# Kernel tuning notes

Hardware: AMD Instinct MI355X
Metric: run time of the kernel (lower is better)

The kernel has to match this reference:

```python
import jax, jax.numpy as jnp
import numpy as np


def setup_inputs() -> dict:
    key = jax.random.key(0)
    k1, k2, k3, k4, k5 = jax.random.split(key, 5)
    B, Di, Dh = 16384, 1024, 1024
    stdv = 1.0 / np.sqrt(Dh)
    return {
        "X": jax.random.normal(k1, (B, Di), dtype=jnp.float32),
        "h0": jax.random.normal(k2, (B, Dh), dtype=jnp.float32),
        "c0": jax.random.normal(k3, (B, Dh), dtype=jnp.float32),
        "U": jax.random.uniform(k4, (Di, 4 * Dh), dtype=jnp.float32, minval=-stdv, maxval=stdv),
        "W": jax.random.uniform(k5, (4 * Dh, Dh), dtype=jnp.float32, minval=-stdv, maxval=stdv),
    }


def reference(X, h0, c0, U, W):
    # Single-step LSTM cell: gates = X @ U + h0 @ W^T, split into i/f/g/o.
    Dh = h0.shape[-1]
    XU = X @ U                      # (B, 4*Dh)
    gates = XU + h0 @ W.T           # (B, 4*Dh)
    i, f, g, o = jnp.split(gates, 4, axis=-1)
    i = jax.nn.sigmoid(i)
    f = jax.nn.sigmoid(f)
    g = jnp.tanh(g)
    o = jax.nn.sigmoid(o)
    c = f * c0 + i * g              # (B, Dh)
    h = o * jnp.tanh(c)             # (B, Dh)
    return (h, c)
```

## Files before the change

kernel.cpp:

```cpp
#include <hip/hip_runtime.h>
#include <hip/hip_bf16.h>
#include <stdint.h>


typedef __bf16 bf16x8 __attribute__((ext_vector_type(8)));
typedef float f32x4 __attribute__((ext_vector_type(4)));

#define B_ROWS 16384
#define KDIM 2048
#define DH 1024
#define HC_ELEMS 16777216ull
#define NT 64

__device__ __forceinline__ unsigned short f2bf(float f) {
  unsigned u = __float_as_uint(f);
  u = (u + 0x7fffu + ((u >> 16) & 1u)) >> 16;
  return (unsigned short)u;
}

__device__ __forceinline__ float fsig(float x) {
  return __builtin_amdgcn_rcpf(1.0f + __expf(-x));
}
__device__ __forceinline__ float ftanh_(float x) {
  return 2.0f * __builtin_amdgcn_rcpf(1.0f + __expf(-2.0f * x)) - 1.0f;
}

__global__ void cast_concat_A(const float* __restrict__ X, const float* __restrict__ h0,
                              unsigned short* __restrict__ A) {
  size_t t = (size_t)blockIdx.x * 256 + threadIdx.x;
  size_t idx = t * 16;
  int m = (int)(idx >> 11);
  int k = (int)(idx & 2047);
  const float* src = (k < 1024) ? (X + (size_t)m * 1024 + k)
                                : (h0 + (size_t)m * 1024 + (k - 1024));
  float4 a = ((const float4*)src)[0];
  float4 b = ((const float4*)src)[1];
  float4 c = ((const float4*)src)[2];
  float4 d = ((const float4*)src)[3];
  union { unsigned short u[16]; uint4 v[2]; } pk;
  pk.u[0] = f2bf(a.x); pk.u[1] = f2bf(a.y); pk.u[2] = f2bf(a.z); pk.u[3] = f2bf(a.w);
  pk.u[4] = f2bf(b.x); pk.u[5] = f2bf(b.y); pk.u[6] = f2bf(b.z); pk.u[7] = f2bf(b.w);
  pk.u[8]  = f2bf(c.x); pk.u[9]  = f2bf(c.y); pk.u[10] = f2bf(c.z); pk.u[11] = f2bf(c.w);
  pk.u[12] = f2bf(d.x); pk.u[13] = f2bf(d.y); pk.u[14] = f2bf(d.z); pk.u[15] = f2bf(d.w);
  *(uint4*)(A + idx) = pk.v[0];
  *(uint4*)(A + idx + 8) = pk.v[1];
}

__global__ void cast_W(const float* __restrict__ W, unsigned short* __restrict__ Bt) {
  size_t t = (size_t)blockIdx.x * 256 + threadIdx.x;
  size_t idx = t * 16;
  int n = (int)(idx >> 10);
  int k = (int)(idx & 1023);
  const float* src = W + (size_t)n * 1024 + k;
  float4 a = ((const float4*)src)[0];
  float4 b = ((const float4*)src)[1];
  float4 c = ((const float4*)src)[2];
  float4 d = ((const float4*)src)[3];
  union { unsigned short u[16]; uint4 v[2]; } pk;
  pk.u[0] = f2bf(a.x); pk.u[1] = f2bf(a.y); pk.u[2] = f2bf(a.z); pk.u[3] = f2bf(a.w);
  pk.u[4] = f2bf(b.x); pk.u[5] = f2bf(b.y); pk.u[6] = f2bf(b.z); pk.u[7] = f2bf(b.w);
  pk.u[8]  = f2bf(c.x); pk.u[9]  = f2bf(c.y); pk.u[10] = f2bf(c.z); pk.u[11] = f2bf(c.w);
  pk.u[12] = f2bf(d.x); pk.u[13] = f2bf(d.y); pk.u[14] = f2bf(d.z); pk.u[15] = f2bf(d.w);
  unsigned short* dst = Bt + (size_t)n * 2048 + 1024 + k;
  *(uint4*)(dst) = pk.v[0];
  *(uint4*)(dst + 8) = pk.v[1];
}

__global__ void transpose_U(const float* __restrict__ U, unsigned short* __restrict__ Bt) {
  __shared__ float tile[32][33];
  int n0 = blockIdx.x * 32;
  int k0 = blockIdx.y * 32;
  int tx = threadIdx.x & 31, ty = threadIdx.x >> 5;
  #pragma unroll
  for (int i = 0; i < 4; ++i)
    tile[ty + i * 8][tx] = U[(size_t)(k0 + ty + i * 8) * 4096 + n0 + tx];
  __syncthreads();
  int nrel = threadIdx.x >> 3;
  int kc = (threadIdx.x & 7) * 4;
  union { unsigned short u[4]; uint2 v8; } pk;
  #pragma unroll
  for (int i = 0; i < 4; ++i) pk.u[i] = f2bf(tile[kc + i][nrel]);
  *(uint2*)(Bt + (size_t)(n0 + nrel) * 2048 + k0 + kc) = pk.v8;
}

__global__ __launch_bounds__(512, 2)
void lstm_gemm(const unsigned short* __restrict__ A, const unsigned short* __restrict__ Bt,
               const float* __restrict__ c0, float* __restrict__ out) {
  extern __shared__ char smem[];
  const int tid = threadIdx.x;
  const int wave = tid >> 6, lane = tid & 63;
  const int q = lane >> 4, cc = lane & 15;
  const int wm = wave >> 2, wn = wave & 3;

  const int bid = blockIdx.x;
  const int swz = (bid & 7) * 128 + (bid >> 3);
  const int m0 = (swz >> 4) * 256;
  const int j0 = (swz & 15) * 64;

  const int srow = lane >> 2;
  const int sseg = (lane & 3) ^ ((lane >> 3) & 3);
  uint32_t aoff[2], boff[2];
  #pragma unroll
  for (int u = 0; u < 2; ++u) {
    int rl = u * 128 + wave * 16 + srow;
    aoff[u] = (((uint32_t)(m0 + rl) << 11) + (uint32_t)(sseg * 8)) * 2u;
    int n = (((rl >> 4) & 3) << 10) + j0 + ((rl >> 6) << 4) + (rl & 15);
    boff[u] = (((uint32_t)n << 11) + (uint32_t)(sseg * 8)) * 2u;
  }
  const char* Ab = (const char*)A;
  const char* Bb = (const char*)Bt;

  auto stageA = [&](int tt, int slot) {
    #pragma unroll
    for (int u = 0; u < 2; ++u) {
      uintptr_t l = (uintptr_t)(smem + slot * 16384 + u * 8192 + wave * 1024);
      __builtin_amdgcn_global_load_lds(
          (const __attribute__((address_space(1))) void*)(uintptr_t)(Ab + (aoff[u] + (uint32_t)tt * 64u)),
          (__attribute__((address_space(3))) void*)(uint32_t)l, 16, 0, 0);
    }
  };
  auto stageB = [&](int tt, int slot) {
    #pragma unroll
    for (int u = 0; u < 2; ++u) {
      uintptr_t l = (uintptr_t)(smem + 65536 + slot * 16384 + u * 8192 + wave * 1024);
      __builtin_amdgcn_global_load_lds(
          (const __attribute__((address_space(1))) void*)(uintptr_t)(Bb + (boff[u] + (uint32_t)tt * 64u)),
          (__attribute__((address_space(3))) void*)(uint32_t)l, 16, 0, 0);
    }
  };

  f32x4 acc[8][4];
  #pragma unroll
  for (int a = 0; a < 8; ++a)
    #pragma unroll
    for (int b = 0; b < 4; ++b)
      acc[a][b] = f32x4{0.f, 0.f, 0.f, 0.f};

  stageA(0, 0); stageB(0, 0);
  stageA(1, 1); stageB(1, 1);
  asm volatile("s_waitcnt vmcnt(4)" ::: "memory");
  __builtin_amdgcn_s_barrier();

  const uint32_t swzq = (uint32_t)((q ^ ((cc >> 1) & 3)) * 16);
  const uint32_t aRd = (uint32_t)((wm * 128 + cc) * 64) + swzq;
  const uint32_t bRd = 65536u + (uint32_t)((wn * 64 + cc) * 64) + swzq;

  for (int t = 0; t < NT; ++t) {
    const char* sbase = smem + (t & 3) * 16384;
    if (t < NT - 2) {
      const int nslot = (t + 2) & 3;
      stageA(t + 2, nslot);
      stageB(t + 2, nslot);
    }
    bf16x8 af[8], bf[4];
    #pragma unroll
    for (int mi = 0; mi < 8; ++mi) af[mi] = *(const bf16x8*)(sbase + aRd + mi * 1024);
    #pragma unroll
    for (int ni = 0; ni < 4; ++ni) bf[ni] = *(const bf16x8*)(sbase + bRd + ni * 1024);
    __builtin_amdgcn_s_setprio(1);
    #pragma unroll
    for (int mi = 0; mi < 8; ++mi)
      #pragma unroll
      for (int ni = 0; ni < 4; ++ni)
        acc[mi][ni] = __builtin_amdgcn_mfma_f32_16x16x32_bf16(af[mi], bf[ni], acc[mi][ni], 0, 0, 0);
    __builtin_amdgcn_s_setprio(0);
    if (t < NT - 2)      asm volatile("s_waitcnt vmcnt(4)" ::: "memory");
    else if (t == NT - 2) asm volatile("s_waitcnt vmcnt(0)" ::: "memory");
    if (t < NT - 1) __builtin_amdgcn_s_barrier();
  }

  const int gj = j0 + wn * 16 + cc;
  #pragma unroll
  for (int mi = 0; mi < 8; ++mi) {
    #pragma unroll
    for (int r = 0; r < 4; ++r) {
      int grow = m0 + wm * 128 + mi * 16 + q * 4 + r;
      float iv = fsig(acc[mi][0][r]);
      float fv = fsig(acc[mi][1][r]);
      float gv = ftanh_(acc[mi][2][r]);
      float ov = fsig(acc[mi][3][r]);
      float c0v = c0[(size_t)grow * DH + gj];
      float cv = fv * c0v + iv * gv;
      float hv = ov * ftanh_(cv);
      out[(size_t)grow * DH + gj] = hv;
      out[HC_ELEMS + (size_t)grow * DH + gj] = cv;
    }
  }
}

extern "C" void kernel_launch(void* const* d_in, const int* in_sizes, int n_in,
                              void* d_out, int out_size, void* d_ws, size_t ws_size,
                              hipStream_t stream) {
  const float* X  = (const float*)d_in[0];
  const float* h0 = (const float*)d_in[1];
  const float* c0 = (const float*)d_in[2];
  const float* U  = (const float*)d_in[3];
  const float* W  = (const float*)d_in[4];
  float* out = (float*)d_out;

  unsigned short* Abf = (unsigned short*)d_ws;
  unsigned short* Bt  = Abf + 33554432ull;

  static bool attr_set = false;
  if (!attr_set) {
    (void)hipFuncSetAttribute(reinterpret_cast<const void*>(lstm_gemm),
                              hipFuncAttributeMaxDynamicSharedMemorySize, 131072);
    attr_set = true;
  }

  cast_concat_A<<<8192, 256, 0, stream>>>(X, h0, Abf);
  cast_W<<<1024, 256, 0, stream>>>(W, Bt);
  transpose_U<<<dim3(128, 32), 256, 0, stream>>>(U, Bt);
  lstm_gemm<<<1024, 512, 131072, stream>>>(Abf, Bt, c0, out);
}
```

Before: 529.8 us.

## Merge prep kernels and double-buffer LDS fragment reads in GEMM loop

The three casting and transposing kernels are merged into one prep launch with a block-index split, which removes two launch gaps. The GEMM main loop is restructured to prefetch three stages ahead and to hold two register fragment sets, so LDS reads for the next k-step overlap the MFMAs of the current one. This raises register pressure (an extra 12 bf16x8 fragments), which could cause spills under the 512x2 launch bounds.

```diff
diff --git a/kernel.cpp b/kernel.cpp
--- a/kernel.cpp
+++ b/kernel.cpp
@@ -25,62 +25,55 @@
   return 2.0f * __builtin_amdgcn_rcpf(1.0f + __expf(-2.0f * x)) - 1.0f;
 }
 
-__global__ void cast_concat_A(const float* __restrict__ X, const float* __restrict__ h0,
-                              unsigned short* __restrict__ A) {
-  size_t t = (size_t)blockIdx.x * 256 + threadIdx.x;
-  size_t idx = t * 16;
-  int m = (int)(idx >> 11);
-  int k = (int)(idx & 2047);
-  const float* src = (k < 1024) ? (X + (size_t)m * 1024 + k)
-                                : (h0 + (size_t)m * 1024 + (k - 1024));
-  float4 a = ((const float4*)src)[0];
-  float4 b = ((const float4*)src)[1];
-  float4 c = ((const float4*)src)[2];
-  float4 d = ((const float4*)src)[3];
-  union { unsigned short u[16]; uint4 v[2]; } pk;
-  pk.u[0] = f2bf(a.x); pk.u[1] = f2bf(a.y); pk.u[2] = f2bf(a.z); pk.u[3] = f2bf(a.w);
-  pk.u[4] = f2bf(b.x); pk.u[5] = f2bf(b.y); pk.u[6] = f2bf(b.z); pk.u[7] = f2bf(b.w);
-  pk.u[8]  = f2bf(c.x); pk.u[9]  = f2bf(c.y); pk.u[10] = f2bf(c.z); pk.u[11] = f2bf(c.w);
-  pk.u[12] = f2bf(d.x); pk.u[13] = f2bf(d.y); pk.u[14] = f2bf(d.z); pk.u[15] = f2bf(d.w);
-  *(uint4*)(A + idx) = pk.v[0];
-  *(uint4*)(A + idx + 8) = pk.v[1];
-}
-
-__global__ void cast_W(const float* __restrict__ W, unsigned short* __restrict__ Bt) {
-  size_t t = (size_t)blockIdx.x * 256 + threadIdx.x;
-  size_t idx = t * 16;
-  int n = (int)(idx >> 10);
-  int k = (int)(idx & 1023);
-  const float* src = W + (size_t)n * 1024 + k;
-  float4 a = ((const float4*)src)[0];
-  float4 b = ((const float4*)src)[1];
-  float4 c = ((const float4*)src)[2];
-  float4 d = ((const float4*)src)[3];
-  union { unsigned short u[16]; uint4 v[2]; } pk;
-  pk.u[0] = f2bf(a.x); pk.u[1] = f2bf(a.y); pk.u[2] = f2bf(a.z); pk.u[3] = f2bf(a.w);
-  pk.u[4] = f2bf(b.x); pk.u[5] = f2bf(b.y); pk.u[6] = f2bf(b.z); pk.u[7] = f2bf(b.w);
-  pk.u[8]  = f2bf(c.x); pk.u[9]  = f2bf(c.y); pk.u[10] = f2bf(c.z); pk.u[11] = f2bf(c.w);
-  pk.u[12] = f2bf(d.x); pk.u[13] = f2bf(d.y); pk.u[14] = f2bf(d.z); pk.u[15] = f2bf(d.w);
-  unsigned short* dst = Bt + (size_t)n * 2048 + 1024 + k;
-  *(uint4*)(dst) = pk.v[0];
-  *(uint4*)(dst + 8) = pk.v[1];
-}
-
-__global__ void transpose_U(const float* __restrict__ U, unsigned short* __restrict__ Bt) {
+__global__ void prep(const float* __restrict__ X, const float* __restrict__ h0,
+                     const float* __restrict__ W, const float* __restrict__ U,
+                     unsigned short* __restrict__ A, unsigned short* __restrict__ Bt) {
   __shared__ float tile[32][33];
-  int n0 = blockIdx.x * 32;
-  int k0 = blockIdx.y * 32;
-  int tx = threadIdx.x & 31, ty = threadIdx.x >> 5;
-  #pragma unroll
-  for (int i = 0; i < 4; ++i)
-    tile[ty + i * 8][tx] = U[(size_t)(k0 + ty + i * 8) * 4096 + n0 + tx];
-  __syncthreads();
-  int nrel = threadIdx.x >> 3;
-  int kc = (threadIdx.x & 7) * 4;
-  union { unsigned short u[4]; uint2 v8; } pk;
-  #pragma unroll
-  for (int i = 0; i < 4; ++i) pk.u[i] = f2bf(tile[kc + i][nrel]);
-  *(uint2*)(Bt + (size_t)(n0 + nrel) * 2048 + k0 + kc) = pk.v8;
+  int b = blockIdx.x;
+  if (b < 9216) {
+    const float* src;
+    unsigned short* dst;
+    if (b < 8192) {
+      size_t idx = ((size_t)b * 256 + threadIdx.x) * 16;
+      int m = (int)(idx >> 11);
+      int k = (int)(idx & 2047);
+      src = (k < 1024) ? (X + (size_t)m * 1024 + k)
+                       : (h0 + (size_t)m * 1024 + (k - 1024));
+      dst = A + idx;
+    } else {
+      size_t idx = ((size_t)(b - 8192) * 256 + threadIdx.x) * 16;
+      int n = (int)(idx >> 10);
+      int k = (int)(idx & 1023);
+      src = W + (size_t)n * 1024 + k;
+      dst = Bt + (size_t)n * 2048 + 1024 + k;
+    }
+    float4 a = ((const float4*)src)[0];
+    float4 bb = ((const float4*)src)[1];
+    float4 c = ((const float4*)src)[2];
+    float4 d = ((const float4*)src)[3];
+    union { unsigned short u[16]; uint4 v[2]; } pk;
+    pk.u[0] = f2bf(a.x); pk.u[1] = f2bf(a.y); pk.u[2] = f2bf(a.z); pk.u[3] = f2bf(a.w);
+    pk.u[4] = f2bf(bb.x); pk.u[5] = f2bf(bb.y); pk.u[6] = f2bf(bb.z); pk.u[7] = f2bf(bb.w);
+    pk.u[8]  = f2bf(c.x); pk.u[9]  = f2bf(c.y); pk.u[10] = f2bf(c.z); pk.u[11] = f2bf(c.w);
+    pk.u[12] = f2bf(d.x); pk.u[13] = f2bf(d.y); pk.u[14] = f2bf(d.z); pk.u[15] = f2bf(d.w);
+    *(uint4*)(dst) = pk.v[0];
+    *(uint4*)(dst + 8) = pk.v[1];
+  } else {
+    int bb = b - 9216;
+    int n0 = (bb & 127) * 32;
+    int k0 = (bb >> 7) * 32;
+    int tx = threadIdx.x & 31, ty = threadIdx.x >> 5;
+    #pragma unroll
+    for (int i = 0; i < 4; ++i)
+      tile[ty + i * 8][tx] = U[(size_t)(k0 + ty + i * 8) * 4096 + n0 + tx];
+    __syncthreads();
+    int nrel = threadIdx.x >> 3;
+    int kc = (threadIdx.x & 7) * 4;
+    union { unsigned short u[4]; uint2 v8; } pk;
+    #pragma unroll
+    for (int i = 0; i < 4; ++i) pk.u[i] = f2bf(tile[kc + i][nrel]);
+    *(uint2*)(Bt + (size_t)(n0 + nrel) * 2048 + k0 + kc) = pk.v8;
+  }
 }
 
 __global__ __launch_bounds__(512, 2)
@@ -110,7 +103,8 @@
   const char* Ab = (const char*)A;
   const char* Bb = (const char*)Bt;
 
-  auto stageA = [&](int tt, int slot) {
+  auto stageAB = [&](int tt) {
+    const int slot = tt & 3;
     #pragma unroll
     for (int u = 0; u < 2; ++u) {
       uintptr_t l = (uintptr_t)(smem + slot * 16384 + u * 8192 + wave * 1024);
@@ -118,8 +112,6 @@
           (const __attribute__((address_space(1))) void*)(uintptr_t)(Ab + (aoff[u] + (uint32_t)tt * 64u)),
           (__attribute__((address_space(3))) void*)(uint32_t)l, 16, 0, 0);
     }
-  };
-  auto stageB = [&](int tt, int slot) {
     #pragma unroll
     for (int u = 0; u < 2; ++u) {
       uintptr_t l = (uintptr_t)(smem + 65536 + slot * 16384 + u * 8192 + wave * 1024);
@@ -136,38 +128,58 @@
     for (int b = 0; b < 4; ++b)
       acc[a][b] = f32x4{0.f, 0.f, 0.f, 0.f};
 
-  stageA(0, 0); stageB(0, 0);
-  stageA(1, 1); stageB(1, 1);
-  asm volatile("s_waitcnt vmcnt(4)" ::: "memory");
-  __builtin_amdgcn_s_barrier();
-
   const uint32_t swzq = (uint32_t)((q ^ ((cc >> 1) & 3)) * 16);
   const uint32_t aRd = (uint32_t)((wm * 128 + cc) * 64) + swzq;
   const uint32_t bRd = 65536u + (uint32_t)((wn * 64 + cc) * 64) + swzq;
 
-  for (int t = 0; t < NT; ++t) {
-    const char* sbase = smem + (t & 3) * 16384;
-    if (t < NT - 2) {
-      const int nslot = (t + 2) & 3;
-      stageA(t + 2, nslot);
-      stageB(t + 2, nslot);
-    }
-    bf16x8 af[8], bf[4];
-    #pragma unroll
-    for (int mi = 0; mi < 8; ++mi) af[mi] = *(const bf16x8*)(sbase + aRd + mi * 1024);
-    #pragma unroll
-    for (int ni = 0; ni < 4; ++ni) bf[ni] = *(const bf16x8*)(sbase + bRd + ni * 1024);
+  auto readFrags = [&](bf16x8 (&fa)[8], bf16x8 (&fb)[4], int slot) {
+    const char* sb = smem + slot * 16384;
+    #pragma unroll
+    for (int mi = 0; mi < 8; ++mi) fa[mi] = *(const bf16x8*)(sb + aRd + mi * 1024);
+    #pragma unroll
+    for (int ni = 0; ni < 4; ++ni) fb[ni] = *(const bf16x8*)(sb + bRd + ni * 1024);
+  };
+  auto domfma = [&](bf16x8 (&fa)[8], bf16x8 (&fb)[4]) {
     __builtin_amdgcn_s_setprio(1);
     #pragma unroll
     for (int mi = 0; mi < 8; ++mi)
       #pragma unroll
       for (int ni = 0; ni < 4; ++ni)
-        acc[mi][ni] = __builtin_amdgcn_mfma_f32_16x16x32_bf16(af[mi], bf[ni], acc[mi][ni], 0, 0, 0);
+        acc[mi][ni] = __builtin_amdgcn_mfma_f32_16x16x32_bf16(fa[mi], fb[ni], acc[mi][ni], 0, 0, 0);
     __builtin_amdgcn_s_setprio(0);
-    if (t < NT - 2)      asm volatile("s_waitcnt vmcnt(4)" ::: "memory");
-    else if (t == NT - 2) asm volatile("s_waitcnt vmcnt(0)" ::: "memory");
-    if (t < NT - 1) __builtin_amdgcn_s_barrier();
-  }
+  };
+
+  stageAB(0); stageAB(1); stageAB(2);
+  asm volatile("s_waitcnt vmcnt(4)" ::: "memory");
+  __builtin_amdgcn_s_barrier();
+
+  bf16x8 a0[8], b0[4], a1[8], b1[4];
+  readFrags(a0, b0, 0);
+
+  for (int t = 0; t < NT - 4; t += 2) {
+    stageAB(t + 3);
+    readFrags(a1, b1, (t + 1) & 3);
+    domfma(a0, b0);
+    asm volatile("s_waitcnt vmcnt(4)" ::: "memory");
+    __builtin_amdgcn_s_barrier();
+    stageAB(t + 4);
+    readFrags(a0, b0, (t + 2) & 3);
+    domfma(a1, b1);
+    asm volatile("s_waitcnt vmcnt(4)" ::: "memory");
+    __builtin_amdgcn_s_barrier();
+  }
+  stageAB(63);
+  readFrags(a1, b1, 61 & 3);
+  domfma(a0, b0);
+  asm volatile("s_waitcnt vmcnt(4)" ::: "memory");
+  __builtin_amdgcn_s_barrier();
+  readFrags(a0, b0, 62 & 3);
+  domfma(a1, b1);
+  asm volatile("s_waitcnt vmcnt(0)" ::: "memory");
+  __builtin_amdgcn_s_barrier();
+  readFrags(a1, b1, 63 & 3);
+  domfma(a0, b0);
+  domfma(a1, b1);
 
   const int gj = j0 + wn * 16 + cc;
   #pragma unroll
@@ -208,8 +220,6 @@
     attr_set = true;
   }
 
-  cast_concat_A<<<8192, 256, 0, stream>>>(X, h0, Abf);
-  cast_W<<<1024, 256, 0, stream>>>(W, Bt);
-  transpose_U<<<dim3(128, 32), 256, 0, stream>>>(U, Bt);
+  prep<<<13312, 256, 0, stream>>>(X, h0, W, U, Abf, Bt);
   lstm_gemm<<<1024, 512, 131072, stream>>>(Abf, Bt, c0, out);
 }
```

After: 546.5 us. +3.1%, slower.
